# Performance work log

Hardware: AMD Instinct MI355X
Metric: run time of the kernel (lower is better)

Reference implementation:

```python
import jax, jax.numpy as jnp
import numpy as np
from jax import lax

B = 12
C1, H1, W1 = 64, 128, 352      # stage1 (stride-4) features
C5, H5, W5 = 512, 64, 176      # stage5 features used for BEV lifting
BEV_H = BEV_W = 128
VOX = 0.4
DC = 48                        # depth bins
MIND, MAXD, MARGIN = 1.0, 60.0, 5.0
PCR = (-51.2, -51.2, -5.0, 51.2, 51.2, 3.0)


def _bn(x, g, b):
    # eval-mode BatchNorm folded to a per-channel affine (running stats folded into g, b)
    return x * g[None, :, None, None] + b[None, :, None, None]


def _conv1x1(x, w):
    return jnp.einsum('bchw,oc->bohw', x, w)


def setup_inputs() -> dict:
    key = jax.random.key(0)
    k = jax.random.split(key, 8)
    stage1 = jax.random.normal(k[0], (B, C1, H1, W1), jnp.float32)
    stage5 = jax.random.normal(k[1], (B, C5, H5, W5), jnp.float32)
    # realistic pinhole intrinsics at stage5 feature resolution
    fx = 80.0
    K = np.array([[fx, 0.0, W5 / 2.0], [0.0, fx, H5 / 2.0], [0.0, 0.0, 1.0]], np.float32)
    intrinsics = jnp.asarray(np.broadcast_to(K, (B, 3, 3)).copy())
    # cam->ego: camera z (depth)->ego x, camera x->-ego y, camera y->-ego z, 1.5 m camera height
    Tm = np.zeros((4, 4), np.float32)
    Tm[0, 2] = 1.0; Tm[1, 0] = -1.0; Tm[2, 1] = -1.0; Tm[2, 3] = 1.5; Tm[3, 3] = 1.0
    extrinsics = jnp.asarray(np.broadcast_to(Tm, (B, 4, 4)).copy())

    def w(kk, shape, s=0.05):
        return jax.random.normal(kk, shape, jnp.float32) * s

    return {
        'stage1': stage1, 'stage5': stage5,
        'intrinsics': intrinsics, 'extrinsics': extrinsics,
        'red1_w': w(k[2], (64, C1)), 'red1_g': jnp.ones((64,), jnp.float32), 'red1_b': jnp.zeros((64,), jnp.float32),
        'skip_w': w(k[3], (32, 64)), 'skip_g': jnp.ones((32,), jnp.float32), 'skip_b': jnp.zeros((32,), jnp.float32),
        'red5_w': w(k[4], (64, C5)), 'red5_g': jnp.ones((64,), jnp.float32), 'red5_b': jnp.zeros((64,), jnp.float32),
        'dep5_w': w(k[5], (DC, C5)), 'dep5_g': jnp.ones((DC,), jnp.float32), 'dep5_b': jnp.zeros((DC,), jnp.float32),
        'main_w': w(k[6], (128, 64, 3, 3)), 'main_g': jnp.ones((128,), jnp.float32), 'main_b': jnp.zeros((128,), jnp.float32),
    }


def reference(stage1, stage5, intrinsics, extrinsics,
              red1_w, red1_g, red1_b, skip_w, skip_g, skip_b,
              red5_w, red5_g, red5_b, dep5_w, dep5_g, dep5_b,
              main_w, main_g, main_b):
    Bn = stage1.shape[0]
    # ---- skip branch (stage1): reduce 1x1 + BN + ReLU, then skip projection ----
    r1 = jax.nn.relu(_bn(_conv1x1(stage1, red1_w), red1_g, red1_b))
    skip = jax.nn.relu(_bn(_conv1x1(r1, skip_w), skip_g, skip_b))
    # ---- stage5 depth-weighted lifting (matches _process_scale) ----
    N = H5 * W5
    yy, xx = jnp.meshgrid(jnp.arange(H5, dtype=jnp.float32), jnp.arange(W5, dtype=jnp.float32), indexing='ij')
    pixels = jnp.stack([xx.ravel(), yy.ravel(), jnp.ones((N,), jnp.float32)], axis=0)  # (3, N)
    reduced = jax.nn.relu(_bn(_conv1x1(stage5, red5_w), red5_g, red5_b)).reshape(Bn, 64, N)
    logits = _bn(_conv1x1(stage5, dep5_w), dep5_g, dep5_b)
    probs = jax.nn.softmax(logits * 10.0, axis=1)                          # (B, DC, H5, W5)
    bins = jnp.exp(jnp.linspace(jnp.log(jnp.float32(MIND)), jnp.log(jnp.float32(MAXD)), DC))
    depth = jnp.clip(jnp.einsum('bdhw,d->bhw', probs, bins), MIND, MAXD + MARGIN).reshape(Bn, 1, N)
    K_inv = jnp.linalg.inv(intrinsics)
    cam = depth * jnp.einsum('bij,jn->bin', K_inv, pixels)                 # (B, 3, N)
    cam_h = jnp.concatenate([cam, jnp.ones((Bn, 1, N), cam.dtype)], axis=1)
    ego = jnp.einsum('bij,bjn->bin', extrinsics, cam_h)[:, :3]             # (B, 3, N)
    ex, ey, ez = ego[:, 0], ego[:, 1], ego[:, 2]
    ego_valid = ((ex >= PCR[0]) & (ex < PCR[3]) & (ey >= PCR[1]) & (ey < PCR[4])
                 & (ez >= PCR[2]) & (ez < PCR[5]))
    bev_x = jnp.floor(ex / VOX + BEV_W // 2).astype(jnp.int32)
    bev_y = jnp.floor(ey / VOX + BEV_H // 2).astype(jnp.int32)
    grid_valid = (bev_x >= 0) & (bev_x < BEV_W) & (bev_y >= 0) & (bev_y < BEV_H)
    valid = grid_valid & ego_valid
    weighted = reduced * jnp.exp(-0.05 * jnp.abs(ez))[:, None, :]
    weighted = jnp.where(valid[:, None, :], weighted, 0.0)                 # (B, 64, N)
    # ---- irregular BEV scatter-add (the kernel-headroom op) ----
    lin = jnp.where(valid, bev_y * BEV_W + bev_x, 0)
    seg = (jnp.arange(Bn, dtype=jnp.int32)[:, None] * (BEV_H * BEV_W) + lin).reshape(-1)
    data = weighted.transpose(0, 2, 1).reshape(Bn * N, 64)
    bev = jax.ops.segment_sum(data, seg, num_segments=Bn * BEV_H * BEV_W)
    bev = bev.reshape(Bn, BEV_H, BEV_W, 64).transpose(0, 3, 1, 2)          # (B, 64, 128, 128)
    # ---- main BEV projection: 3x3 conv + BN + ReLU ----
    out = lax.conv_general_dilated(bev, main_w, (1, 1), ((1, 1), (1, 1)),
                                   dimension_numbers=('NCHW', 'OIHW', 'NCHW'))
    out = jax.nn.relu(_bn(out, main_g, main_b))
    return (out, skip)
```

## Files before the change

### kernel.cpp

```cpp
#include <hip/hip_runtime.h>
#include <math.h>

#define BB 12
#define C1 64
#define H1 128
#define W1 352
#define HW1 (H1*W1)
#define C5 512
#define H5 64
#define W5 176
#define N5 (H5*W5)
#define BEVH 128
#define BEVW 128
#define BEVHW (BEVH*BEVW)
#define DCH 48

#define OFF_W1T   0
#define OFF_WST   4096
#define OFF_W5T   6144
#define OFF_WDT   38912
#define OFF_WMT   63488
#define OFF_BINS  137216
#define OFF_KINV  137264

#define OUT_SZ ((size_t)BB*128*BEVHW)

__global__ void prep_kernel(const float* __restrict__ r1w, const float* __restrict__ r1g,
                            const float* __restrict__ skw, const float* __restrict__ skg,
                            const float* __restrict__ r5w, const float* __restrict__ r5g,
                            const float* __restrict__ dpw, const float* __restrict__ dpg,
                            const float* __restrict__ mw,  const float* __restrict__ mg,
                            const float* __restrict__ intr, float* __restrict__ ws)
{
    int t = blockIdx.x*blockDim.x + threadIdx.x;
    int stride = gridDim.x*blockDim.x;
    for (int i=t; i<64*64; i+=stride){ int c=i>>6, o=i&63;  ws[OFF_W1T + c*64+o] = r1w[o*64+c]*r1g[o]; }
    for (int i=t; i<64*32; i+=stride){ int c=i>>5, s=i&31;  ws[OFF_WST + c*32+s] = skw[s*64+c]*skg[s]; }
    for (int i=t; i<512*64; i+=stride){ int c=i>>6, o=i&63; ws[OFF_W5T + c*64+o] = r5w[o*512+c]*r5g[o]; }
    for (int i=t; i<512*48; i+=stride){ int c=i/48, d=i-c*48; ws[OFF_WDT + c*48+d] = dpw[d*512+c]*dpg[d]; }
    for (int i=t; i<9*64*128; i+=stride){
        int o=i&127; int rest=i>>7; int c=rest&63; int tap=rest>>6; int dy=tap/3, dx=tap-dy*3;
        ws[OFF_WMT + i] = mw[((o*64+c)*3+dy)*3+dx]*mg[o];
    }
    for (int i=t; i<DCH; i+=stride){ ws[OFF_BINS+i] = expf(logf(60.0f)*(float)i/47.0f); }
    for (int i=t; i<BB; i+=stride){
        const float* K = intr + i*9;
        float a=K[0],b=K[1],c=K[2],d=K[3],e=K[4],f=K[5],g=K[6],h=K[7],k=K[8];
        float det = a*(e*k-f*h) - b*(d*k-f*g) + c*(d*h-e*g);
        float id = 1.0f/det;
        float* o_ = ws + OFF_KINV + i*9;
        o_[0]=(e*k-f*h)*id; o_[1]=(c*h-b*k)*id; o_[2]=(b*f-c*e)*id;
        o_[3]=(f*g-d*k)*id; o_[4]=(a*k-c*g)*id; o_[5]=(c*d-a*f)*id;
        o_[6]=(d*h-e*g)*id; o_[7]=(b*g-a*h)*id; o_[8]=(a*e-b*d)*id;
    }
}

__global__ __launch_bounds__(256) void kA(const float* __restrict__ s1, const float* __restrict__ ws,
                                          const float* __restrict__ b1, const float* __restrict__ bsk,
                                          float* __restrict__ outskip)
{
    int p = blockIdx.x*256 + threadIdx.x;
    if (p >= BB*HW1) return;
    int b = p / HW1; int hw = p - b*HW1;
    const float* x  = s1 + (size_t)b*C1*HW1 + hw;
    const float* w1 = ws + OFF_W1T;
    float y[64];
    #pragma unroll
    for (int o=0;o<64;o++) y[o]=0.f;
    #pragma unroll 2
    for (int c=0;c<64;c++){
        float v = x[(size_t)c*HW1];
        const float* wr = w1 + c*64;
        #pragma unroll
        for (int o=0;o<64;o++) y[o] += v*wr[o];
    }
    #pragma unroll
    for (int o=0;o<64;o++) y[o] = fmaxf(y[o]+b1[o], 0.f);
    float s[32];
    #pragma unroll
    for (int i=0;i<32;i++) s[i]=0.f;
    const float* w2 = ws + OFF_WST;
    #pragma unroll 2
    for (int o=0;o<64;o++){
        float v = y[o];
        const float* wr = w2 + o*32;
        #pragma unroll
        for (int i=0;i<32;i++) s[i] += v*wr[i];
    }
    float* op = outskip + (size_t)b*32*HW1 + hw;
    #pragma unroll
    for (int i=0;i<32;i++) op[(size_t)i*HW1] = fmaxf(s[i]+bsk[i], 0.f);
}

__global__ __launch_bounds__(256) void kB(const float* __restrict__ s5, const float* __restrict__ ws,
                                          const float* __restrict__ b5, const float* __restrict__ bd,
                                          const float* __restrict__ extr, float* __restrict__ bev)
{
    int p = blockIdx.x*256 + threadIdx.x;
    if (p >= BB*N5) return;
    int b = p / N5; int n = p - b*N5;
    const float* x  = s5 + (size_t)b*C5*N5 + n;
    const float* w5 = ws + OFF_W5T;
    const float* wd = ws + OFF_WDT;
    float aR[64], aD[48];
    #pragma unroll
    for (int o=0;o<64;o++) aR[o]=0.f;
    #pragma unroll
    for (int d=0;d<48;d++) aD[d]=0.f;
    #pragma unroll 2
    for (int c=0;c<512;c++){
        float v = x[(size_t)c*N5];
        const float* wr = w5 + c*64;
        const float* wq = wd + c*48;
        #pragma unroll
        for (int o=0;o<64;o++) aR[o] += v*wr[o];
        #pragma unroll
        for (int d=0;d<48;d++) aD[d] += v*wq[d];
    }
    #pragma unroll
    for (int o=0;o<64;o++) aR[o] = fmaxf(aR[o]+b5[o], 0.f);
    float m = -1e30f;
    #pragma unroll
    for (int d=0;d<48;d++){ aD[d] = (aD[d]+bd[d])*10.f; m = fmaxf(m, aD[d]); }
    float sum=0.f, dsum=0.f;
    const float* bins = ws + OFF_BINS;
    #pragma unroll
    for (int d=0;d<48;d++){ float e = expf(aD[d]-m); sum += e; dsum += e*bins[d]; }
    float depth = dsum/sum;
    depth = fminf(fmaxf(depth, 1.0f), 65.0f);

    float px = (float)(n - (n/W5)*W5);
    float py = (float)(n / W5);
    const float* Ki = ws + OFF_KINV + b*9;
    float cx = depth*(Ki[0]*px + Ki[1]*py + Ki[2]);
    float cy = depth*(Ki[3]*px + Ki[4]*py + Ki[5]);
    float cz = depth*(Ki[6]*px + Ki[7]*py + Ki[8]);
    const float* E = extr + b*16;
    float ex = E[0]*cx + E[1]*cy + E[2]*cz  + E[3];
    float ey = E[4]*cx + E[5]*cy + E[6]*cz  + E[7];
    float ez = E[8]*cx + E[9]*cy + E[10]*cz + E[11];
    bool valid = (ex >= -51.2f) && (ex < 51.2f) && (ey >= -51.2f) && (ey < 51.2f)
              && (ez >= -5.0f)  && (ez < 3.0f);
    int bx = (int)floorf(ex/0.4f + 64.0f);
    int by = (int)floorf(ey/0.4f + 64.0f);
    valid = valid && (bx>=0) && (bx<BEVW) && (by>=0) && (by<BEVH);
    if (valid){
        float wgt = expf(-0.05f*fabsf(ez));
        float* bp = bev + (size_t)b*64*BEVHW + (size_t)by*BEVW + bx;
        #pragma unroll
        for (int o=0;o<64;o++) atomicAdd(bp + (size_t)o*BEVHW, aR[o]*wgt);
    }
}

__global__ __launch_bounds__(128) void kC(const float* __restrict__ bev, const float* __restrict__ ws,
                                          const float* __restrict__ bm, float* __restrict__ out)
{
    int x = threadIdx.x;
    int y = blockIdx.x;
    int bz = blockIdx.y;
    int b = bz >> 1; int obase = (bz & 1) * 64;
    const float* bp = bev + (size_t)b*64*BEVHW;
    float acc[64];
    #pragma unroll
    for (int o=0;o<64;o++) acc[o]=0.f;
    for (int dy=0; dy<3; dy++){
        int yy = y + dy - 1;
        if (yy < 0 || yy >= BEVH) continue;
        for (int dx=0; dx<3; dx++){
            int xx = x + dx - 1;
            bool ok = (xx >= 0) && (xx < BEVW);
            int xc = min(max(xx,0), BEVW-1);
            const float* wt = ws + OFF_WMT + (size_t)((dy*3+dx)*64)*128 + obase;
            const float* ip = bp + (size_t)yy*BEVW + xc;
            #pragma unroll 2
            for (int c=0;c<64;c++){
                float v = ip[(size_t)c*BEVHW];
                v = ok ? v : 0.f;
                const float* wr = wt + c*128;
                #pragma unroll
                for (int o=0;o<64;o++) acc[o] += v*wr[o];
            }
        }
    }
    float* op = out + (size_t)b*128*BEVHW + (size_t)obase*BEVHW + (size_t)y*BEVW + x;
    #pragma unroll
    for (int o=0;o<64;o++) op[(size_t)o*BEVHW] = fmaxf(acc[o] + bm[obase+o], 0.f);
}

extern "C" void kernel_launch(void* const* d_in, const int* in_sizes, int n_in,
                              void* d_out, int out_size, void* d_ws, size_t ws_size,
                              hipStream_t stream)
{
    const float* stage1 = (const float*)d_in[0];
    const float* stage5 = (const float*)d_in[1];
    const float* intr   = (const float*)d_in[2];
    const float* extr   = (const float*)d_in[3];
    const float* r1w=(const float*)d_in[4];  const float* r1g=(const float*)d_in[5];  const float* r1b=(const float*)d_in[6];
    const float* skw=(const float*)d_in[7];  const float* skg=(const float*)d_in[8];  const float* skb=(const float*)d_in[9];
    const float* r5w=(const float*)d_in[10]; const float* r5g=(const float*)d_in[11]; const float* r5b=(const float*)d_in[12];
    const float* dpw=(const float*)d_in[13]; const float* dpg=(const float*)d_in[14]; const float* dpb=(const float*)d_in[15];
    const float* mw =(const float*)d_in[16]; const float* mg =(const float*)d_in[17]; const float* mb =(const float*)d_in[18];

    float* out  = (float*)d_out;
    float* skip = out + OUT_SZ;
    float* ws   = (float*)d_ws;
    float* bev  = skip;

    prep_kernel<<<dim3(544), dim3(256), 0, stream>>>(r1w,r1g,skw,skg,r5w,r5g,dpw,dpg,mw,mg,intr,ws);
    hipMemsetAsync(bev, 0, (size_t)BB*64*BEVHW*sizeof(float), stream);
    kB<<<dim3((BB*N5+255)/256), dim3(256), 0, stream>>>(stage5, ws, r5b, dpb, extr, bev);
    kC<<<dim3(128, BB*2), dim3(128), 0, stream>>>(bev, ws, mb, out);
    kA<<<dim3((BB*HW1+255)/256), dim3(256), 0, stream>>>(stage1, ws, r1b, skb, skip);
}
```

Before: 1.392 ms.

## Split depth/projection pass from feature reduction to skip invalid pixels

The fused stage5 kernel is split in two. The first pass computes only the depth head, softmax and projection, and stores a BEV index and weight per pixel. The second pass runs the 512-to-64 reduction only for pixels whose index is valid, then scatters with atomics. This avoids the reduction for pixels that fall outside the BEV grid and lowers register pressure in each kernel, at the cost of reading stage5 twice and writing small index and weight buffers into the skip output region before kA overwrites it.

```diff
diff --git a/kernel.cpp b/kernel.cpp
--- a/kernel.cpp
+++ b/kernel.cpp
@@ -23,7 +23,9 @@
 #define OFF_BINS  137216
 #define OFF_KINV  137264
 
-#define OUT_SZ ((size_t)BB*128*BEVHW)
+#define OUT_SZ     ((size_t)BB*128*BEVHW)
+#define BEV_FLOATS ((size_t)BB*64*BEVHW)
+#define NPIX       (BB*N5)
 
 __global__ void prep_kernel(const float* __restrict__ r1w, const float* __restrict__ r1g,
                             const float* __restrict__ skw, const float* __restrict__ skg,
@@ -92,33 +94,25 @@
     for (int i=0;i<32;i++) op[(size_t)i*HW1] = fmaxf(s[i]+bsk[i], 0.f);
 }
 
-__global__ __launch_bounds__(256) void kB(const float* __restrict__ s5, const float* __restrict__ ws,
-                                          const float* __restrict__ b5, const float* __restrict__ bd,
-                                          const float* __restrict__ extr, float* __restrict__ bev)
+__global__ __launch_bounds__(256) void kB1(const float* __restrict__ s5, const float* __restrict__ ws,
+                                           const float* __restrict__ bd, const float* __restrict__ extr,
+                                           int* __restrict__ idxb, float* __restrict__ wgtb)
 {
     int p = blockIdx.x*256 + threadIdx.x;
-    if (p >= BB*N5) return;
+    if (p >= NPIX) return;
     int b = p / N5; int n = p - b*N5;
     const float* x  = s5 + (size_t)b*C5*N5 + n;
-    const float* w5 = ws + OFF_W5T;
     const float* wd = ws + OFF_WDT;
-    float aR[64], aD[48];
-    #pragma unroll
-    for (int o=0;o<64;o++) aR[o]=0.f;
+    float aD[48];
     #pragma unroll
     for (int d=0;d<48;d++) aD[d]=0.f;
-    #pragma unroll 2
+    #pragma unroll 4
     for (int c=0;c<512;c++){
         float v = x[(size_t)c*N5];
-        const float* wr = w5 + c*64;
         const float* wq = wd + c*48;
         #pragma unroll
-        for (int o=0;o<64;o++) aR[o] += v*wr[o];
-        #pragma unroll
         for (int d=0;d<48;d++) aD[d] += v*wq[d];
     }
-    #pragma unroll
-    for (int o=0;o<64;o++) aR[o] = fmaxf(aR[o]+b5[o], 0.f);
     float m = -1e30f;
     #pragma unroll
     for (int d=0;d<48;d++){ aD[d] = (aD[d]+bd[d])*10.f; m = fmaxf(m, aD[d]); }
@@ -144,12 +138,37 @@
     int bx = (int)floorf(ex/0.4f + 64.0f);
     int by = (int)floorf(ey/0.4f + 64.0f);
     valid = valid && (bx>=0) && (bx<BEVW) && (by>=0) && (by<BEVH);
-    if (valid){
-        float wgt = expf(-0.05f*fabsf(ez));
-        float* bp = bev + (size_t)b*64*BEVHW + (size_t)by*BEVW + bx;
-        #pragma unroll
-        for (int o=0;o<64;o++) atomicAdd(bp + (size_t)o*BEVHW, aR[o]*wgt);
-    }
+    idxb[p] = valid ? (by*BEVW + bx) : -1;
+    wgtb[p] = expf(-0.05f*fabsf(ez));
+}
+
+__global__ __launch_bounds__(256) void kB2(const float* __restrict__ s5, const float* __restrict__ ws,
+                                           const float* __restrict__ b5,
+                                           const int* __restrict__ idxb, const float* __restrict__ wgtb,
+                                           float* __restrict__ bev)
+{
+    int p = blockIdx.x*256 + threadIdx.x;
+    if (p >= NPIX) return;
+    int lin = idxb[p];
+    if (lin < 0) return;
+    int b = p / N5; int n = p - b*N5;
+    const float* x  = s5 + (size_t)b*C5*N5 + n;
+    const float* w5 = ws + OFF_W5T;
+    float aR[64];
+    #pragma unroll
+    for (int o=0;o<64;o++) aR[o]=0.f;
+    #pragma unroll 4
+    for (int c=0;c<512;c++){
+        float v = x[(size_t)c*N5];
+        const float* wr = w5 + c*64;
+        #pragma unroll
+        for (int o=0;o<64;o++) aR[o] += v*wr[o];
+    }
+    float wgt = wgtb[p];
+    float* bp = bev + (size_t)b*64*BEVHW + lin;
+    #pragma unroll
+    for (int o=0;o<64;o++)
+        atomicAdd(bp + (size_t)o*BEVHW, fmaxf(aR[o]+b5[o], 0.f)*wgt);
 }
 
 __global__ __launch_bounds__(128) void kC(const float* __restrict__ bev, const float* __restrict__ ws,
@@ -205,10 +224,13 @@
     float* skip = out + OUT_SZ;
     float* ws   = (float*)d_ws;
     float* bev  = skip;
+    int*   idxb = (int*)(skip + BEV_FLOATS);
+    float* wgtb = skip + BEV_FLOATS + NPIX;
 
     prep_kernel<<<dim3(544), dim3(256), 0, stream>>>(r1w,r1g,skw,skg,r5w,r5g,dpw,dpg,mw,mg,intr,ws);
-    hipMemsetAsync(bev, 0, (size_t)BB*64*BEVHW*sizeof(float), stream);
-    kB<<<dim3((BB*N5+255)/256), dim3(256), 0, stream>>>(stage5, ws, r5b, dpb, extr, bev);
+    hipMemsetAsync(bev, 0, BEV_FLOATS*sizeof(float), stream);
+    kB1<<<dim3((NPIX+255)/256), dim3(256), 0, stream>>>(stage5, ws, dpb, extr, idxb, wgtb);
+    kB2<<<dim3((NPIX+255)/256), dim3(256), 0, stream>>>(stage5, ws, r5b, idxb, wgtb, bev);
     kC<<<dim3(128, BB*2), dim3(128), 0, stream>>>(bev, ws, mb, out);
     kA<<<dim3((BB*HW1+255)/256), dim3(256), 0, stream>>>(stage1, ws, r1b, skb, skip);
 }
```

Result: no change. 1.404 ms (+0.9%).
